# Kernel tuning notes

Measured on AMD Instinct MI355X. Metric: run time of the kernel, lower is better.

The kernel has to match this reference:

```python
import jax, jax.numpy as jnp
import numpy as np

N_NODES = 50000
N_EDGES = 640000
DIM_IN = 128
DIM_OUT = 32
HEADS = 4
NEG_SLOPE = 0.2


def setup_inputs() -> dict:
    key = jax.random.key(0)
    ks = jax.random.split(key, 8)
    HC = HEADS * DIM_OUT
    x = jax.random.normal(ks[0], (N_NODES, DIM_IN), dtype=jnp.float32)
    edge_index = jax.random.randint(ks[1], (2, N_EDGES), 0, N_NODES, dtype=jnp.int32)
    s = 1.0 / np.sqrt(DIM_IN)
    Wl = jax.random.normal(ks[2], (DIM_IN, HC), dtype=jnp.float32) * s   # lin_l (source)
    Wr = jax.random.normal(ks[3], (DIM_IN, HC), dtype=jnp.float32) * s   # lin_r (target)
    att = jax.random.normal(ks[4], (HEADS, DIM_OUT), dtype=jnp.float32) * (1.0 / np.sqrt(DIM_OUT))
    bias = jnp.zeros((HC,), dtype=jnp.float32)
    Wp = jax.random.normal(ks[5], (HC, DIM_OUT), dtype=jnp.float32) * (1.0 / np.sqrt(HC))
    bp = jnp.zeros((DIM_OUT,), dtype=jnp.float32)
    return {"x": x, "edge_index": edge_index, "Wl": Wl, "Wr": Wr,
            "att": att, "bias": bias, "Wp": Wp, "bp": bp}


def reference(x, edge_index, Wl, Wr, att, bias, Wp, bp):
    N = x.shape[0]
    H, C = att.shape
    src = edge_index[0]  # j: message source
    dst = edge_index[1]  # i: message target (softmax segment)
    xl = (x @ Wl).reshape(N, H, C)  # source-side transform
    xr = (x @ Wr).reshape(N, H, C)  # target-side transform
    # GATv2: e_ij = a^T LeakyReLU(xl_j + xr_i)
    e = jax.nn.leaky_relu(xl[src] + xr[dst], NEG_SLOPE)        # [E,H,C]
    logits = jnp.einsum('ehc,hc->eh', e, att)                  # [E,H]
    m = jax.ops.segment_max(logits, dst, num_segments=N)       # [N,H]
    ex = jnp.exp(logits - m[dst])
    denom = jax.ops.segment_sum(ex, dst, num_segments=N)       # [N,H]
    alpha = ex / (denom[dst] + 1e-16)                          # [E,H]
    msg = xl[src] * alpha[:, :, None]                          # [E,H,C]
    out = jax.ops.segment_sum(msg, dst, num_segments=N)        # [N,H,C]
    out = out.reshape(N, H * C) + bias                         # concat heads + bias
    return out @ Wp + bp                                       # proj to dim_out
```

## Files before the change

### kernel.cpp

```cpp
#include <hip/hip_runtime.h>
#include <hip/hip_bf16.h>
#include <math.h>

#define N_NODES 50000
#define N_EDGES 640000
#define HEADS 4
#define CDIM 32
#define HC 128
#define DIN 128
#define DOUT 32
#define NEG_SLOPE 0.2f
#define TPAD 136
#define BCAP 64
#define NPB 16
#define EPT 16
#define ZERO_NB ((N_NODES + 255) / 256)
#define WT_NB (2 * DIN * HC / 256)
#define WPT_NB (DOUT * HC / 256)
#define FILL_NB ((N_EDGES + 256 * EPT - 1) / (256 * EPT))
#define TF_NB ((N_NODES + 63) / 64)

typedef __hip_bfloat16 bf16;
typedef __attribute__((ext_vector_type(8))) short short8;
typedef __attribute__((ext_vector_type(4))) float floatx4;
typedef __attribute__((ext_vector_type(4))) unsigned short ushort4v;

static __device__ __forceinline__ float bflo(unsigned w) { return __uint_as_float(w << 16); }
static __device__ __forceinline__ float bfhi(unsigned w) { return __uint_as_float(w & 0xFFFF0000u); }
static __device__ __forceinline__ unsigned short f2bf(float f) {
    union { bf16 h; unsigned short u; } cv; cv.h = __float2bfloat16(f); return cv.u;
}

__global__ __launch_bounds__(256) void k_prep(
    unsigned* __restrict__ cnt,
    const float* __restrict__ Wl, const float* __restrict__ Wr,
    const float* __restrict__ bias, const float* __restrict__ Wp,
    const float* __restrict__ bp,
    bf16* __restrict__ WlF, bf16* __restrict__ WrF, bf16* __restrict__ WpT,
    float* __restrict__ cvec)
{
    const int t = threadIdx.x, b = blockIdx.x;
    if (b < ZERO_NB) {
        const int i = b * 256 + t;
        if (i < N_NODES) cnt[i] = 0u;
    } else if (b < ZERO_NB + WT_NB) {
        const int i = (b - ZERO_NB) * 256 + t;
        const int i2 = (i < DIN * HC) ? i : i - DIN * HC;
        const int c = i2 >> 7, j = i2 & 127;
        const int jt = j >> 4, m = j & 15;
        const int kk = c >> 5, quad = (c >> 3) & 3, u = c & 7;
        const int idx = (jt * 4 + kk) * 512 + (quad * 16 + m) * 8 + u;
        if (i < DIN * HC) WlF[idx] = __float2bfloat16(Wl[i2]);
        else              WrF[idx] = __float2bfloat16(Wr[i2]);
    } else if (b < ZERO_NB + WT_NB + WPT_NB) {
        const int i = (b - ZERO_NB - WT_NB) * 256 + t;
        const int c = i >> 5, j = i & 31;
        WpT[j * HC + c] = __float2bfloat16(Wp[i]);
    } else if (t < DOUT) {
        float v = bp[t];
        for (int c = 0; c < HC; c++) v += bias[c] * Wp[c * DOUT + t];
        cvec[t] = v;
    }
}

__global__ __launch_bounds__(256) void k_fill(
    const int* __restrict__ ei, unsigned* __restrict__ cnt,
    int* __restrict__ srcs)
{
    const int e0 = (blockIdx.x * 256 + threadIdx.x) * EPT;
    if (e0 >= N_EDGES) return;
    if (e0 + EPT <= N_EDGES) {
        int s[EPT], d[EPT];
        #pragma unroll
        for (int q = 0; q < EPT / 4; q++) {
            const int4 sv = *(const int4*)(ei + e0 + q * 4);
            const int4 dv = *(const int4*)(ei + N_EDGES + e0 + q * 4);
            s[q * 4] = sv.x; s[q * 4 + 1] = sv.y; s[q * 4 + 2] = sv.z; s[q * 4 + 3] = sv.w;
            d[q * 4] = dv.x; d[q * 4 + 1] = dv.y; d[q * 4 + 2] = dv.z; d[q * 4 + 3] = dv.w;
        }
        unsigned pos[EPT];
        #pragma unroll
        for (int i = 0; i < EPT; i++)
            pos[i] = atomicAdd(&cnt[d[i]], 1u);
        #pragma unroll
        for (int i = 0; i < EPT; i++)
            if (pos[i] < BCAP) srcs[((size_t)d[i] << 6) + pos[i]] = s[i];
    } else {
        for (int i = 0; i < EPT && e0 + i < N_EDGES; i++) {
            const int dd = ei[N_EDGES + e0 + i];
            const unsigned pos = atomicAdd(&cnt[dd], 1u);
            if (pos < BCAP) srcs[((size_t)dd << 6) + pos] = ei[e0 + i];
        }
    }
}

__global__ __launch_bounds__(256) void k_tf(
    const float* __restrict__ x,
    const bf16* __restrict__ WlF, const bf16* __restrict__ WrF,
    bf16* __restrict__ xl, bf16* __restrict__ xr)
{
    const int t = threadIdx.x, b = blockIdx.x;
    const int n0 = b * 64;
    const int w = t >> 6, lane = t & 63;
    const int m = lane & 15, quad = lane >> 4;
    const int node = n0 + w * 16 + m;
    const bool valid = (node < N_NODES);

    const float* xrow = x + (size_t)(valid ? node : 0) * DIN;
    short8 af[4];
    #pragma unroll
    for (int kk = 0; kk < 4; kk++) {
        const float4 lo = *(const float4*)(xrow + kk * 32 + quad * 8);
        const float4 hi = *(const float4*)(xrow + kk * 32 + quad * 8 + 4);
        short8 v;
        v[0] = (short)f2bf(lo.x); v[1] = (short)f2bf(lo.y);
        v[2] = (short)f2bf(lo.z); v[3] = (short)f2bf(lo.w);
        v[4] = (short)f2bf(hi.x); v[5] = (short)f2bf(hi.y);
        v[6] = (short)f2bf(hi.z); v[7] = (short)f2bf(hi.w);
        af[kk] = v;
    }

    const short8* wlf = (const short8*)WlF;
    const short8* wrf = (const short8*)WrF;
    #pragma unroll
    for (int jt = 0; jt < 8; jt++) {
        floatx4 aL = {0.f, 0.f, 0.f, 0.f};
        floatx4 aR = {0.f, 0.f, 0.f, 0.f};
        #pragma unroll
        for (int kk = 0; kk < 4; kk++) {
            const short8 bl = wlf[(jt * 4 + kk) * 64 + lane];
            const short8 br = wrf[(jt * 4 + kk) * 64 + lane];
            aL = __builtin_amdgcn_mfma_f32_16x16x32_bf16(bl, af[kk], aL, 0, 0, 0);
            aR = __builtin_amdgcn_mfma_f32_16x16x32_bf16(br, af[kk], aR, 0, 0, 0);
        }
        if (valid) {
            ushort4v pl, pr;
            #pragma unroll
            for (int r = 0; r < 4; r++) {
                pl[r] = f2bf(aL[r]);
                pr[r] = f2bf(aR[r]);
            }
            *(ushort4v*)(xl + (size_t)node * HC + jt * 16 + quad * 4) = pl;
            *(ushort4v*)(xr + (size_t)node * HC + jt * 16 + quad * 4) = pr;
        }
    }
}

__global__ __launch_bounds__(256) void k_agg(
    const int* __restrict__ srcs, const unsigned* __restrict__ cnt,
    const unsigned* __restrict__ xl2,
    const unsigned* __restrict__ xr2,
    const float* __restrict__ att,
    const bf16* __restrict__ WpT,
    const float* __restrict__ cvec,
    float* __restrict__ out)
{
    __shared__ __align__(16) unsigned short srow[NPB][TPAD];
    const int t = threadIdx.x;
    const int w = t >> 6, lane = t & 63;
    const int es = lane >> 4, hq = lane & 15;

    const float4 av0 = ((const float4*)att)[hq * 2];
    const float4 av1 = ((const float4*)att)[hq * 2 + 1];
    const float a_[8] = {av0.x, av0.y, av0.z, av0.w, av1.x, av1.y, av1.z, av1.w};

    for (int ni = 0; ni < 4; ni++) {
        const int node = blockIdx.x * NPB + w * 4 + ni;

        const uint4 xru = ((const uint4*)(xr2 + (size_t)node * 64))[hq];
        float xr_[8];
        xr_[0] = bflo(xru.x); xr_[1] = bfhi(xru.x);
        xr_[2] = bflo(xru.y); xr_[3] = bfhi(xru.y);
        xr_[4] = bflo(xru.z); xr_[5] = bfhi(xru.z);
        xr_[6] = bflo(xru.w); xr_[7] = bfhi(xru.w);

        unsigned cn = cnt[node]; if (cn > BCAP) cn = BCAP;
        const unsigned lo = (unsigned)node << 6, hi = lo + cn;
        float s_run = 0.f;
        float acc[8] = {0.f, 0.f, 0.f, 0.f, 0.f, 0.f, 0.f, 0.f};

        for (unsigned base = lo; base < hi; base += 64) {
            const unsigned j = base + lane;
            const int srcj = (j < hi) ? srcs[j] : 0;
            const int cnt2 = (int)((hi - base < 64u) ? (hi - base) : 64u);
            int sj = __shfl(srcj, es, 64);
            uint4 xa = ((const uint4*)(xl2 + ((size_t)((es < cnt2) ? sj : 0) << 6)))[hq];
            sj = __shfl(srcj, (es + 4) & 63, 64);
            uint4 xb = ((const uint4*)(xl2 + ((size_t)((es + 4 < cnt2) ? sj : 0) << 6)))[hq];
            for (int i = 0; i < cnt2; i += 8) {
                #pragma unroll
                for (int u = 0; u < 2; u++) {
                    const int eidx = i + es + 4 * u;
                    const uint4 cur = u ? xb : xa;
                    const int ii = eidx + 8;
                    sj = __shfl(srcj, ii & 63, 64);
                    const uint4 nxt = ((const uint4*)(xl2 + ((size_t)((ii < cnt2) ? sj : 0) << 6)))[hq];
                    if (u) xb = nxt; else xa = nxt;

                    float x_[8];
                    x_[0] = bflo(cur.x); x_[1] = bfhi(cur.x);
                    x_[2] = bflo(cur.y); x_[3] = bfhi(cur.y);
                    x_[4] = bflo(cur.z); x_[5] = bfhi(cur.z);
                    x_[6] = bflo(cur.w); x_[7] = bfhi(cur.w);
                    float p = 0.f;
                    #pragma unroll
                    for (int k = 0; k < 8; k++) {
                        float v = x_[k] + xr_[k];
                        v = fmaxf(v, NEG_SLOPE * v);
                        p = fmaf(a_[k], v, p);
                    }
                    p += __shfl_xor(p, 1, 64);
                    p += __shfl_xor(p, 2, 64);
                    const float e_ = (eidx < cnt2) ? __expf(p) : 0.f;
                    s_run += e_;
                    #pragma unroll
                    for (int k = 0; k < 8; k++) acc[k] = fmaf(x_[k], e_, acc[k]);
                }
            }
        }
        s_run += __shfl_xor(s_run, 16, 64);
        s_run += __shfl_xor(s_run, 32, 64);
        #pragma unroll
        for (int k = 0; k < 8; k++) {
            acc[k] += __shfl_xor(acc[k], 16, 64);
            acc[k] += __shfl_xor(acc[k], 32, 64);
        }
        const float rden = 1.f / (s_run + 1e-16f);

        if (es == 0) {
            union { unsigned short s[8]; uint4 v; } pk;
            #pragma unroll
            for (int k = 0; k < 8; k++) pk.s[k] = f2bf(acc[k] * rden);
            *(uint4*)&srow[w * 4 + ni][hq * 8] = pk.v;
        }
    }
    __syncthreads();

    if (w < 2) {
        const int m = lane & 15, quad = lane >> 4;
        short8 af[4];
        #pragma unroll
        for (int kk = 0; kk < 4; kk++)
            af[kk] = *(const short8*)&srow[m][kk * 32 + quad * 8];
        floatx4 d = {0.f, 0.f, 0.f, 0.f};
        #pragma unroll
        for (int kk = 0; kk < 4; kk++) {
            const short8 bfr = *(const short8*)(WpT + (w * 16 + m) * HC + kk * 32 + quad * 8);
            d = __builtin_amdgcn_mfma_f32_16x16x32_bf16(af[kk], bfr, d, 0, 0, 0);
        }
        const int jj = w * 16 + m;
        const float cv = cvec[jj];
        #pragma unroll
        for (int r = 0; r < 4; r++) {
            const int node = blockIdx.x * NPB + quad * 4 + r;
            out[(size_t)node * DOUT + jj] = d[r] + cv;
        }
    }
}

extern "C" void kernel_launch(void* const* d_in, const int* in_sizes, int n_in,
                              void* d_out, int out_size, void* d_ws, size_t ws_size,
                              hipStream_t stream)
{
    const float* x    = (const float*)d_in[0];
    const int*   ei   = (const int*)d_in[1];
    const float* Wl   = (const float*)d_in[2];
    const float* Wr   = (const float*)d_in[3];
    const float* att  = (const float*)d_in[4];
    const float* bias = (const float*)d_in[5];
    const float* Wp   = (const float*)d_in[6];
    const float* bp   = (const float*)d_in[7];
    float* out = (float*)d_out;

    bf16* xl       = (bf16*)d_ws;
    bf16* xr       = xl + (size_t)N_NODES * HC;
    bf16* WlF      = xr + (size_t)N_NODES * HC;
    bf16* WrF      = WlF + DIN * HC;
    bf16* WpT      = WrF + DIN * HC;
    float* cvec    = (float*)(WpT + DOUT * HC);
    unsigned* cnt  = (unsigned*)(cvec + DOUT);
    int* srcs      = (int*)(cnt + N_NODES);

    k_prep<<<ZERO_NB + WT_NB + WPT_NB + 1, 256, 0, stream>>>(
        cnt, Wl, Wr, bias, Wp, bp, WlF, WrF, WpT, cvec);
    k_fill<<<FILL_NB, 256, 0, stream>>>(ei, cnt, srcs);
    k_tf<<<TF_NB, 256, 0, stream>>>(x, WlF, WrF, xl, xr);
    k_agg<<<N_NODES / NPB, 256, 0, stream>>>(srcs, cnt,
        (const unsigned*)xl, (const unsigned*)xr, att, WpT, cvec, out);
}
```

Before: 177.6 us.

## Deepen gather prefetch in aggregation, hoist per-node loads, retile transform and fill

The aggregation kernel now loads the counts, source lists and xr rows for all four nodes of a wave up front, then keeps four gathered xl rows in flight instead of two. This should hide more of the random-gather latency. The transform kernel handles two 16-node tiles per wave so the weight fragments are reused across twice as many nodes. The fill kernel drops to 4 edges per thread with no tail handling, which relies on the edge count being divisible by 1024. Register pressure rises, and unused srcs slots are read without masking when a node has fewer than 64 edges, though those values are then ignored.

```diff
diff --git a/kernel.cpp b/kernel.cpp
--- a/kernel.cpp
+++ b/kernel.cpp
@@ -13,12 +13,12 @@
 #define TPAD 136
 #define BCAP 64
 #define NPB 16
-#define EPT 16
+#define EPT 4
 #define ZERO_NB ((N_NODES + 255) / 256)
 #define WT_NB (2 * DIN * HC / 256)
 #define WPT_NB (DOUT * HC / 256)
-#define FILL_NB ((N_EDGES + 256 * EPT - 1) / (256 * EPT))
-#define TF_NB ((N_NODES + 63) / 64)
+#define FILL_NB (N_EDGES / (256 * EPT))
+#define TF_NB ((N_NODES + 127) / 128)
 
 typedef __hip_bfloat16 bf16;
 typedef __attribute__((ext_vector_type(8))) short short8;
@@ -68,30 +68,17 @@
     int* __restrict__ srcs)
 {
     const int e0 = (blockIdx.x * 256 + threadIdx.x) * EPT;
-    if (e0 >= N_EDGES) return;
-    if (e0 + EPT <= N_EDGES) {
-        int s[EPT], d[EPT];
-        #pragma unroll
-        for (int q = 0; q < EPT / 4; q++) {
-            const int4 sv = *(const int4*)(ei + e0 + q * 4);
-            const int4 dv = *(const int4*)(ei + N_EDGES + e0 + q * 4);
-            s[q * 4] = sv.x; s[q * 4 + 1] = sv.y; s[q * 4 + 2] = sv.z; s[q * 4 + 3] = sv.w;
-            d[q * 4] = dv.x; d[q * 4 + 1] = dv.y; d[q * 4 + 2] = dv.z; d[q * 4 + 3] = dv.w;
-        }
-        unsigned pos[EPT];
-        #pragma unroll
-        for (int i = 0; i < EPT; i++)
-            pos[i] = atomicAdd(&cnt[d[i]], 1u);
-        #pragma unroll
-        for (int i = 0; i < EPT; i++)
-            if (pos[i] < BCAP) srcs[((size_t)d[i] << 6) + pos[i]] = s[i];
-    } else {
-        for (int i = 0; i < EPT && e0 + i < N_EDGES; i++) {
-            const int dd = ei[N_EDGES + e0 + i];
-            const unsigned pos = atomicAdd(&cnt[dd], 1u);
-            if (pos < BCAP) srcs[((size_t)dd << 6) + pos] = ei[e0 + i];
-        }
-    }
+    const int4 sv = *(const int4*)(ei + e0);
+    const int4 dv = *(const int4*)(ei + N_EDGES + e0);
+    const int s[4] = {sv.x, sv.y, sv.z, sv.w};
+    const int d[4] = {dv.x, dv.y, dv.z, dv.w};
+    unsigned pos[4];
+    #pragma unroll
+    for (int i = 0; i < EPT; i++)
+        pos[i] = atomicAdd(&cnt[d[i]], 1u);
+    #pragma unroll
+    for (int i = 0; i < EPT; i++)
+        if (pos[i] < BCAP) srcs[((size_t)d[i] << 6) + pos[i]] = s[i];
 }
 
 __global__ __launch_bounds__(256) void k_tf(
@@ -100,50 +87,100 @@
     bf16* __restrict__ xl, bf16* __restrict__ xr)
 {
     const int t = threadIdx.x, b = blockIdx.x;
-    const int n0 = b * 64;
+    const int n0 = b * 128;
     const int w = t >> 6, lane = t & 63;
     const int m = lane & 15, quad = lane >> 4;
-    const int node = n0 + w * 16 + m;
-    const bool valid = (node < N_NODES);
-
-    const float* xrow = x + (size_t)(valid ? node : 0) * DIN;
-    short8 af[4];
+    const int na = n0 + w * 32 + m;
+    const int nb = na + 16;
+    const bool va = (na < N_NODES), vb = (nb < N_NODES);
+
+    const float* xpa = x + (size_t)(va ? na : 0) * DIN;
+    const float* xpb = x + (size_t)(vb ? nb : 0) * DIN;
+    short8 afa[4], afb[4];
     #pragma unroll
     for (int kk = 0; kk < 4; kk++) {
-        const float4 lo = *(const float4*)(xrow + kk * 32 + quad * 8);
-        const float4 hi = *(const float4*)(xrow + kk * 32 + quad * 8 + 4);
-        short8 v;
-        v[0] = (short)f2bf(lo.x); v[1] = (short)f2bf(lo.y);
-        v[2] = (short)f2bf(lo.z); v[3] = (short)f2bf(lo.w);
-        v[4] = (short)f2bf(hi.x); v[5] = (short)f2bf(hi.y);
-        v[6] = (short)f2bf(hi.z); v[7] = (short)f2bf(hi.w);
-        af[kk] = v;
+        const float4 la = *(const float4*)(xpa + kk * 32 + quad * 8);
+        const float4 ha = *(const float4*)(xpa + kk * 32 + quad * 8 + 4);
+        const float4 lb = *(const float4*)(xpb + kk * 32 + quad * 8);
+        const float4 hb = *(const float4*)(xpb + kk * 32 + quad * 8 + 4);
+        short8 va8, vb8;
+        va8[0] = (short)f2bf(la.x); va8[1] = (short)f2bf(la.y);
+        va8[2] = (short)f2bf(la.z); va8[3] = (short)f2bf(la.w);
+        va8[4] = (short)f2bf(ha.x); va8[5] = (short)f2bf(ha.y);
+        va8[6] = (short)f2bf(ha.z); va8[7] = (short)f2bf(ha.w);
+        vb8[0] = (short)f2bf(lb.x); vb8[1] = (short)f2bf(lb.y);
+        vb8[2] = (short)f2bf(lb.z); vb8[3] = (short)f2bf(lb.w);
+        vb8[4] = (short)f2bf(hb.x); vb8[5] = (short)f2bf(hb.y);
+        vb8[6] = (short)f2bf(hb.z); vb8[7] = (short)f2bf(hb.w);
+        afa[kk] = va8;
+        afb[kk] = vb8;
     }
 
     const short8* wlf = (const short8*)WlF;
     const short8* wrf = (const short8*)WrF;
     #pragma unroll
     for (int jt = 0; jt < 8; jt++) {
-        floatx4 aL = {0.f, 0.f, 0.f, 0.f};
-        floatx4 aR = {0.f, 0.f, 0.f, 0.f};
+        floatx4 aLa = {0.f,0.f,0.f,0.f}, aLb = {0.f,0.f,0.f,0.f};
+        floatx4 aRa = {0.f,0.f,0.f,0.f}, aRb = {0.f,0.f,0.f,0.f};
         #pragma unroll
         for (int kk = 0; kk < 4; kk++) {
             const short8 bl = wlf[(jt * 4 + kk) * 64 + lane];
             const short8 br = wrf[(jt * 4 + kk) * 64 + lane];
-            aL = __builtin_amdgcn_mfma_f32_16x16x32_bf16(bl, af[kk], aL, 0, 0, 0);
-            aR = __builtin_amdgcn_mfma_f32_16x16x32_bf16(br, af[kk], aR, 0, 0, 0);
-        }
-        if (valid) {
+            aLa = __builtin_amdgcn_mfma_f32_16x16x32_bf16(bl, afa[kk], aLa, 0, 0, 0);
+            aLb = __builtin_amdgcn_mfma_f32_16x16x32_bf16(bl, afb[kk], aLb, 0, 0, 0);
+            aRa = __builtin_amdgcn_mfma_f32_16x16x32_bf16(br, afa[kk], aRa, 0, 0, 0);
+            aRb = __builtin_amdgcn_mfma_f32_16x16x32_bf16(br, afb[kk], aRb, 0, 0, 0);
+        }
+        const int joff = jt * 16 + quad * 4;
+        if (va) {
             ushort4v pl, pr;
             #pragma unroll
-            for (int r = 0; r < 4; r++) {
-                pl[r] = f2bf(aL[r]);
-                pr[r] = f2bf(aR[r]);
-            }
-            *(ushort4v*)(xl + (size_t)node * HC + jt * 16 + quad * 4) = pl;
-            *(ushort4v*)(xr + (size_t)node * HC + jt * 16 + quad * 4) = pr;
-        }
-    }
+            for (int r = 0; r < 4; r++) { pl[r] = f2bf(aLa[r]); pr[r] = f2bf(aRa[r]); }
+            *(ushort4v*)(xl + (size_t)na * HC + joff) = pl;
+            *(ushort4v*)(xr + (size_t)na * HC + joff) = pr;
+        }
+        if (vb) {
+            ushort4v pl, pr;
+            #pragma unroll
+            for (int r = 0; r < 4; r++) { pl[r] = f2bf(aLb[r]); pr[r] = f2bf(aRb[r]); }
+            *(ushort4v*)(xl + (size_t)nb * HC + joff) = pl;
+            *(ushort4v*)(xr + (size_t)nb * HC + joff) = pr;
+        }
+    }
+}
+
+static __device__ __forceinline__ uint4 gat(
+    const int srcj, const int e, const int cn,
+    const unsigned* __restrict__ xl2, const int hq)
+{
+    const int s = __shfl(srcj, e & 63, 64);
+    const size_t row = (size_t)((e < cn) ? s : 0) << 6;
+    return ((const uint4*)(xl2 + row))[hq];
+}
+
+static __device__ __forceinline__ void consume_edge(
+    const uint4 bx, const int eidx, const int cn,
+    const float* __restrict__ xr_, const float* __restrict__ a_,
+    float& s_run, float* __restrict__ acc)
+{
+    float x_[8];
+    x_[0] = bflo(bx.x); x_[1] = bfhi(bx.x);
+    x_[2] = bflo(bx.y); x_[3] = bfhi(bx.y);
+    x_[4] = bflo(bx.z); x_[5] = bfhi(bx.z);
+    x_[6] = bflo(bx.w); x_[7] = bfhi(bx.w);
+    float p = 0.f;
+    #pragma unroll
+    for (int k = 0; k < 8; k++) {
+        float v = x_[k] + xr_[k];
+        v = fmaxf(v, NEG_SLOPE * v);
+        p = fmaf(a_[k], v, p);
+    }
+    p += __shfl_xor(p, 1, 64);
+    p += __shfl_xor(p, 2, 64);
+    const float e_ = (eidx < cn) ? __expf(p) : 0.f;
+    s_run += e_;
+    #pragma unroll
+    for (int k = 0; k < 8; k++) acc[k] = fmaf(x_[k], e_, acc[k]);
 }
 
 __global__ __launch_bounds__(256) void k_agg(
@@ -164,59 +201,47 @@
     const float4 av1 = ((const float4*)att)[hq * 2 + 1];
     const float a_[8] = {av0.x, av0.y, av0.z, av0.w, av1.x, av1.y, av1.z, av1.w};
 
+    const int nb0 = blockIdx.x * NPB + w * 4;
+    const uint4 cv4 = *(const uint4*)(cnt + nb0);
+    int cns[4];
+    cns[0] = (int)(cv4.x < 64u ? cv4.x : 64u);
+    cns[1] = (int)(cv4.y < 64u ? cv4.y : 64u);
+    cns[2] = (int)(cv4.z < 64u ? cv4.z : 64u);
+    cns[3] = (int)(cv4.w < 64u ? cv4.w : 64u);
+    int srcjv[4];
+    uint4 xru[4];
+    #pragma unroll
     for (int ni = 0; ni < 4; ni++) {
-        const int node = blockIdx.x * NPB + w * 4 + ni;
-
-        const uint4 xru = ((const uint4*)(xr2 + (size_t)node * 64))[hq];
+        srcjv[ni] = srcs[((size_t)(nb0 + ni) << 6) + lane];
+        xru[ni] = ((const uint4*)(xr2 + (size_t)(nb0 + ni) * 64))[hq];
+    }
+
+    #pragma unroll
+    for (int ni = 0; ni < 4; ni++) {
+        const int cn = cns[ni];
         float xr_[8];
-        xr_[0] = bflo(xru.x); xr_[1] = bfhi(xru.x);
-        xr_[2] = bflo(xru.y); xr_[3] = bfhi(xru.y);
-        xr_[4] = bflo(xru.z); xr_[5] = bfhi(xru.z);
-        xr_[6] = bflo(xru.w); xr_[7] = bfhi(xru.w);
-
-        unsigned cn = cnt[node]; if (cn > BCAP) cn = BCAP;
-        const unsigned lo = (unsigned)node << 6, hi = lo + cn;
+        xr_[0] = bflo(xru[ni].x); xr_[1] = bfhi(xru[ni].x);
+        xr_[2] = bflo(xru[ni].y); xr_[3] = bfhi(xru[ni].y);
+        xr_[4] = bflo(xru[ni].z); xr_[5] = bfhi(xru[ni].z);
+        xr_[6] = bflo(xru[ni].w); xr_[7] = bfhi(xru[ni].w);
         float s_run = 0.f;
         float acc[8] = {0.f, 0.f, 0.f, 0.f, 0.f, 0.f, 0.f, 0.f};
-
-        for (unsigned base = lo; base < hi; base += 64) {
-            const unsigned j = base + lane;
-            const int srcj = (j < hi) ? srcs[j] : 0;
-            const int cnt2 = (int)((hi - base < 64u) ? (hi - base) : 64u);
-            int sj = __shfl(srcj, es, 64);
-            uint4 xa = ((const uint4*)(xl2 + ((size_t)((es < cnt2) ? sj : 0) << 6)))[hq];
-            sj = __shfl(srcj, (es + 4) & 63, 64);
-            uint4 xb = ((const uint4*)(xl2 + ((size_t)((es + 4 < cnt2) ? sj : 0) << 6)))[hq];
-            for (int i = 0; i < cnt2; i += 8) {
-                #pragma unroll
-                for (int u = 0; u < 2; u++) {
-                    const int eidx = i + es + 4 * u;
-                    const uint4 cur = u ? xb : xa;
-                    const int ii = eidx + 8;
-                    sj = __shfl(srcj, ii & 63, 64);
-                    const uint4 nxt = ((const uint4*)(xl2 + ((size_t)((ii < cnt2) ? sj : 0) << 6)))[hq];
-                    if (u) xb = nxt; else xa = nxt;
-
-                    float x_[8];
-                    x_[0] = bflo(cur.x); x_[1] = bfhi(cur.x);
-                    x_[2] = bflo(cur.y); x_[3] = bfhi(cur.y);
-                    x_[4] = bflo(cur.z); x_[5] = bfhi(cur.z);
-                    x_[6] = bflo(cur.w); x_[7] = bfhi(cur.w);
-                    float p = 0.f;
-                    #pragma unroll
-                    for (int k = 0; k < 8; k++) {
-                        float v = x_[k] + xr_[k];
-                        v = fmaxf(v, NEG_SLOPE * v);
-                        p = fmaf(a_[k], v, p);
-                    }
-                    p += __shfl_xor(p, 1, 64);
-                    p += __shfl_xor(p, 2, 64);
-                    const float e_ = (eidx < cnt2) ? __expf(p) : 0.f;
-                    s_run += e_;
-                    #pragma unroll
-                    for (int k = 0; k < 8; k++) acc[k] = fmaf(x_[k], e_, acc[k]);
-                }
-            }
+        const int sj = srcjv[ni];
+
+        uint4 b0 = gat(sj, es,      cn, xl2, hq);
+        uint4 b1 = gat(sj, es + 4,  cn, xl2, hq);
+        uint4 b2 = gat(sj, es + 8,  cn, xl2, hq);
+        uint4 b3 = gat(sj, es + 12, cn, xl2, hq);
+        for (int i = 0; i < cn; i += 16) {
+            const bool more = (i + 16 < cn);
+            consume_edge(b0, i + es,      cn, xr_, a_, s_run, acc);
+            if (more) b0 = gat(sj, i + 16 + es, cn, xl2, hq);
+            consume_edge(b1, i + es + 4,  cn, xr_, a_, s_run, acc);
+            if (more) b1 = gat(sj, i + 20 + es, cn, xl2, hq);
+            consume_edge(b2, i + es + 8,  cn, xr_, a_, s_run, acc);
+            if (more) b2 = gat(sj, i + 24 + es, cn, xl2, hq);
+            consume_edge(b3, i + es + 12, cn, xr_, a_, s_run, acc);
+            if (more) b3 = gat(sj, i + 28 + es, cn, xl2, hq);
         }
         s_run += __shfl_xor(s_run, 16, 64);
         s_run += __shfl_xor(s_run, 32, 64);
```

Result: faster. 171.5 us (-3.5%).
